# Performance work log

Hardware: AMD Instinct MI355X
Metric: run time of the kernel (lower is better)

The kernel has to match this reference:

```python
import jax, jax.numpy as jnp
import numpy as np

# Phi-3-small blocksparse config
S = 2048            # num prompt tokens (single sequence)
H = 32              # num query heads
HKV = 8             # num kv heads (GQA)
D = 128             # head size
BLK = 64            # sparse_block_size
LOCAL = 16          # local_blocks
VERT = 8            # vert_stride
SCALE = 0.08838834764831845  # 1/sqrt(128)
HEAD_SLIDE = max(1, VERT // H)  # = 1 (per-head vertical offset, homo_head=False)


def _blocksparse_mask():
    """Per-head local+strided block-sparse causal mask, shape [H, S, S] bool."""
    nb = S // BLK
    qb = jnp.arange(nb)[None, :, None]   # query block idx
    kb = jnp.arange(nb)[None, None, :]   # key block idx
    h = jnp.arange(H)[:, None, None]
    blk = (qb >= kb) & (
        (qb - kb < LOCAL) | (((kb + h * HEAD_SLIDE + 1) % VERT) == 0)
    )  # [H, nb, nb]
    dense = jnp.repeat(jnp.repeat(blk, BLK, axis=1), BLK, axis=2)  # [H, S, S]
    causal = jnp.arange(S)[:, None] >= jnp.arange(S)[None, :]
    return dense & causal[None]


def setup_inputs() -> dict:
    key = jax.random.key(0)
    k1, k2, k3 = jax.random.split(key, 3)
    return {
        "query": jax.random.normal(k1, (S, H * D), dtype=jnp.float32),
        "key": jax.random.normal(k2, (S, HKV * D), dtype=jnp.float32),
        "value": jax.random.normal(k3, (S, HKV * D), dtype=jnp.float32),
    }


def reference(query, key, value):
    q = query.reshape(S, H, D)
    k = jnp.repeat(key.reshape(S, HKV, D), H // HKV, axis=1)    # GQA expand
    v = jnp.repeat(value.reshape(S, HKV, D), H // HKV, axis=1)
    scores = jnp.einsum("qhd,khd->hqk", q, k) * SCALE           # [H, S, S]
    mask = _blocksparse_mask()
    scores = jnp.where(mask, scores, jnp.finfo(scores.dtype).min)
    p = jax.nn.softmax(scores, axis=-1)
    out = jnp.einsum("hqk,khd->qhd", p, v)                      # [S, H, D]
    return out.reshape(S, H * D)
```

## Files before the change

kernel.cpp:

```cpp
#include <hip/hip_runtime.h>


typedef __bf16 bf16_t;
typedef __bf16 bf16x4 __attribute__((ext_vector_type(4)));
typedef __bf16 bf16x8 __attribute__((ext_vector_type(8)));
typedef float  fx4    __attribute__((ext_vector_type(4)));

#define SL2E_F 0.1275240614354876f

__device__ inline void load_lds16(const bf16_t* g, bf16_t* l) {
    __builtin_amdgcn_global_load_lds(
        (const __attribute__((address_space(1))) void*)g,
        (__attribute__((address_space(3))) void*)l, 16, 0, 0);
}

__global__ void prep_kernel(const float* __restrict__ K, const float* __restrict__ V,
                            bf16_t* __restrict__ Kb, bf16_t* __restrict__ VT)
{
    const int blk = blockIdx.x;
    {
        const size_t base = (size_t)blk * 4096 + (size_t)threadIdx.x * 16;
        fx4 a0 = *(const fx4*)(K + base);
        fx4 a1 = *(const fx4*)(K + base + 4);
        fx4 a2 = *(const fx4*)(K + base + 8);
        fx4 a3 = *(const fx4*)(K + base + 12);
        bf16x8 f0, f1;
        f0[0]=(bf16_t)a0[0]; f0[1]=(bf16_t)a0[1]; f0[2]=(bf16_t)a0[2]; f0[3]=(bf16_t)a0[3];
        f0[4]=(bf16_t)a1[0]; f0[5]=(bf16_t)a1[1]; f0[6]=(bf16_t)a1[2]; f0[7]=(bf16_t)a1[3];
        f1[0]=(bf16_t)a2[0]; f1[1]=(bf16_t)a2[1]; f1[2]=(bf16_t)a2[2]; f1[3]=(bf16_t)a2[3];
        f1[4]=(bf16_t)a3[0]; f1[5]=(bf16_t)a3[1]; f1[6]=(bf16_t)a3[2]; f1[7]=(bf16_t)a3[3];
        *(bf16x8*)(Kb + base)     = f0;
        *(bf16x8*)(Kb + base + 8) = f1;
    }
    __shared__ __align__(16) bf16_t T[64 * 72];
    const int s0 = (blk & 31) * 64;
    const int c0 = (blk >> 5) * 64;
    const int tx = threadIdx.x & 15, ty = threadIdx.x >> 4;
    fx4 a0 = *(const fx4*)(V + (size_t)(s0 + ty * 4 + 0) * 1024 + c0 + tx * 4);
    fx4 a1 = *(const fx4*)(V + (size_t)(s0 + ty * 4 + 1) * 1024 + c0 + tx * 4);
    fx4 a2 = *(const fx4*)(V + (size_t)(s0 + ty * 4 + 2) * 1024 + c0 + tx * 4);
    fx4 a3 = *(const fx4*)(V + (size_t)(s0 + ty * 4 + 3) * 1024 + c0 + tx * 4);
#pragma unroll
    for (int j = 0; j < 4; ++j) {
        bf16x4 f = { (bf16_t)a0[j], (bf16_t)a1[j], (bf16_t)a2[j], (bf16_t)a3[j] };
        *(bf16x4*)&T[(tx * 4 + j) * 72 + ty * 4] = f;
    }
    __syncthreads();
    const int c = threadIdx.x >> 2, part = threadIdx.x & 3;
    bf16x8 x0 = *(const bf16x8*)&T[c * 72 + part * 16];
    bf16x8 x1 = *(const bf16x8*)&T[c * 72 + part * 16 + 8];
    bf16_t* dst = VT + (size_t)(c0 + c) * 2048 + s0 + part * 16;
    *(bf16x8*)(dst)     = x0;
    *(bf16x8*)(dst + 8) = x1;
}

__launch_bounds__(128, 2)
__global__ void bsfa_kernel(const float* __restrict__ Q,
                            const bf16_t* __restrict__ Kb,
                            const bf16_t* __restrict__ VT,
                            float* __restrict__ O)
{
    const int blk  = blockIdx.x;
    const int kvh  = blk & 7;
    const int h    = kvh * 4 + ((blk >> 3) & 3);
    const int qb   = 31 - (blk >> 5);
    const int tid  = threadIdx.x;
    const int rh   = tid >> 6;
    const int lane = tid & 63;
    const int l15  = lane & 15;
    const int quad = lane >> 4;

    __shared__ __align__(16) bf16_t Ks[64 * 128];
    __shared__ __align__(16) bf16_t Vs[128 * 64];

    bf16_t* Pt = &Ks[rh * 2304];

    const int row0 = qb * 64 + rh * 32;

    const bf16_t* kg = Kb + (size_t)kvh * 128;
    const bf16_t* vg = VT + ((size_t)kvh * 128) * 2048;

    bf16x8 qf[2][4];
#pragma unroll
    for (int qt = 0; qt < 2; ++qt) {
        const float* qp = Q + (size_t)(row0 + qt * 16 + l15) * 4096 + h * 128;
#pragma unroll
        for (int kc = 0; kc < 4; ++kc) {
            fx4 a = *(const fx4*)(qp + kc * 32 + quad * 8);
            fx4 b = *(const fx4*)(qp + kc * 32 + quad * 8 + 4);
            bf16x8 f;
            f[0] = (bf16_t)(a[0] * SL2E_F); f[1] = (bf16_t)(a[1] * SL2E_F);
            f[2] = (bf16_t)(a[2] * SL2E_F); f[3] = (bf16_t)(a[3] * SL2E_F);
            f[4] = (bf16_t)(b[0] * SL2E_F); f[5] = (bf16_t)(b[1] * SL2E_F);
            f[6] = (bf16_t)(b[2] * SL2E_F); f[7] = (bf16_t)(b[3] * SL2E_F);
            qf[qt][kc] = f;
        }
    }

    bf16x8 ones;
#pragma unroll
    for (int i = 0; i < 8; ++i) ones[i] = (bf16_t)1.0f;

    fx4 oacc[8][2];
    fx4 lacc[2];
    const fx4 zero4 = {0.0f, 0.0f, 0.0f, 0.0f};
#pragma unroll
    for (int dt = 0; dt < 8; ++dt)
#pragma unroll
        for (int qt = 0; qt < 2; ++qt)
            oacc[dt][qt] = zero4;
    lacc[0] = zero4; lacc[1] = zero4;

    for (int kb = 0; kb <= qb; ++kb) {
        if (!((qb - kb < 16) || (((kb + h + 1) & 7) == 0))) continue;

        {
            const bf16_t* kt_g = kg + ((size_t)kb << 16);
            const bf16_t* vt_g = vg + ((size_t)kb << 6);
#pragma unroll
            for (int i = 0; i < 8; ++i) {
                const int chunk = i * 128 + tid;
                const int krow = chunk >> 4;
                const int kc   = (chunk & 15) ^ (krow & 15);
                load_lds16(kt_g + (size_t)krow * 1024 + kc * 8, Ks + (size_t)chunk * 8);
                const int vrow = chunk >> 3;
                const int vc   = (chunk & 7) ^ (vrow & 7);
                load_lds16(vt_g + (size_t)vrow * 2048 + vc * 8, Vs + (size_t)chunk * 8);
            }
        }
        __syncthreads();

        fx4 sacc[4][2];
#pragma unroll
        for (int kt = 0; kt < 4; ++kt)
#pragma unroll
            for (int qt = 0; qt < 2; ++qt)
                sacc[kt][qt] = zero4;
#pragma unroll
        for (int kc = 0; kc < 4; ++kc)
#pragma unroll
            for (int kt = 0; kt < 4; ++kt) {
                bf16x8 kf = *(const bf16x8*)&Ks[(kt * 16 + l15) * 128 + (((kc * 4 + quad) ^ l15)) * 8];
#pragma unroll
                for (int qt = 0; qt < 2; ++qt)
                    sacc[kt][qt] = __builtin_amdgcn_mfma_f32_16x16x32_bf16(
                        kf, qf[qt][kc], sacc[kt][qt], 0, 0, 0);
            }

        if (kb == qb) {
#pragma unroll
            for (int kt = 0; kt < 4; ++kt)
#pragma unroll
                for (int qt = 0; qt < 2; ++qt)
#pragma unroll
                    for (int r = 0; r < 4; ++r) {
                        const int k_in = kt * 16 + quad * 4 + r;
                        const int q_in = rh * 32 + qt * 16 + l15;
                        if (q_in < k_in) sacc[kt][qt][r] = -1e30f;
                    }
        }

#pragma unroll
        for (int kt = 0; kt < 4; ++kt)
#pragma unroll
            for (int qt = 0; qt < 2; ++qt)
#pragma unroll
                for (int r = 0; r < 4; ++r)
                    sacc[kt][qt][r] = exp2f(sacc[kt][qt][r]);

        __syncthreads();

#pragma unroll
        for (int qt = 0; qt < 2; ++qt)
#pragma unroll
            for (int kt = 0; kt < 4; ++kt) {
                bf16x4 f = { (bf16_t)sacc[kt][qt][0], (bf16_t)sacc[kt][qt][1],
                             (bf16_t)sacc[kt][qt][2], (bf16_t)sacc[kt][qt][3] };
                *(bf16x4*)&Pt[(qt * 16 + l15) * 72 + kt * 16 + quad * 4] = f;
            }
        __asm__ __volatile__("s_waitcnt lgkmcnt(0)" ::: "memory");

        bf16x8 pf[2][2];
#pragma unroll
        for (int qt = 0; qt < 2; ++qt)
#pragma unroll
            for (int kcg = 0; kcg < 2; ++kcg)
                pf[qt][kcg] = *(const bf16x8*)&Pt[(qt * 16 + l15) * 72 + kcg * 32 + quad * 8];

#pragma unroll
        for (int kcg = 0; kcg < 2; ++kcg) {
#pragma unroll
            for (int dt = 0; dt < 8; ++dt) {
                bf16x8 vf = *(const bf16x8*)&Vs[(dt * 16 + l15) * 64 + (((kcg * 4 + quad) ^ (l15 & 7))) * 8];
#pragma unroll
                for (int qt = 0; qt < 2; ++qt)
                    oacc[dt][qt] = __builtin_amdgcn_mfma_f32_16x16x32_bf16(
                        vf, pf[qt][kcg], oacc[dt][qt], 0, 0, 0);
            }
#pragma unroll
            for (int qt = 0; qt < 2; ++qt)
                lacc[qt] = __builtin_amdgcn_mfma_f32_16x16x32_bf16(
                    ones, pf[qt][kcg], lacc[qt], 0, 0, 0);
        }

        __syncthreads();
    }

    const float inv0 = 1.0f / lacc[0][0];
    const float inv1 = 1.0f / lacc[1][0];
#pragma unroll
    for (int dt = 0; dt < 8; ++dt)
#pragma unroll
        for (int qt = 0; qt < 2; ++qt) {
            const float inv = qt ? inv1 : inv0;
            fx4 o = oacc[dt][qt] * inv;
            *(fx4*)(O + (size_t)(row0 + qt * 16 + l15) * 4096 + h * 128 + dt * 16 + quad * 4) = o;
        }
}

extern "C" void kernel_launch(void* const* d_in, const int* in_sizes, int n_in,
                              void* d_out, int out_size, void* d_ws, size_t ws_size,
                              hipStream_t stream) {
    (void)in_sizes; (void)n_in; (void)ws_size; (void)out_size;
    const float* q = (const float*)d_in[0];
    const float* k = (const float*)d_in[1];
    const float* v = (const float*)d_in[2];
    float* o = (float*)d_out;

    bf16_t* Kb = (bf16_t*)d_ws;
    bf16_t* VT = Kb + (size_t)2048 * 1024;

    prep_kernel<<<dim3(512), dim3(256), 0, stream>>>(k, v, Kb, VT);
    bsfa_kernel<<<dim3(1024), dim3(128), 0, stream>>>(q, Kb, VT, o);
}
```

Before: 138.7 us.

## Share K/V tiles across four load-balanced query blocks with double-buffered LDS

Each workgroup now has four waves, each owning a full 64-row query block chosen as x, 15-x, 16+x, 31-x so causal work is balanced. K/V tiles for the union of needed key blocks are staged once into double-buffered LDS and prefetched ahead of compute, which cuts redundant global loads. The P operand is rearranged in registers with permlane swaps instead of an LDS round trip. In exchange the grid drops to 256 workgroups with heavy register use (larger accumulators), which risks low occupancy and idle waves on tiles another wave needs.

```diff
diff --git a/kernel.cpp b/kernel.cpp
--- a/kernel.cpp
+++ b/kernel.cpp
@@ -5,6 +5,8 @@
 typedef __bf16 bf16x4 __attribute__((ext_vector_type(4)));
 typedef __bf16 bf16x8 __attribute__((ext_vector_type(8)));
 typedef float  fx4    __attribute__((ext_vector_type(4)));
+typedef unsigned u32x2 __attribute__((ext_vector_type(2)));
+typedef unsigned u32x4 __attribute__((ext_vector_type(4)));
 
 #define SL2E_F 0.1275240614354876f
 
@@ -12,6 +14,17 @@
     __builtin_amdgcn_global_load_lds(
         (const __attribute__((address_space(1))) void*)g,
         (__attribute__((address_space(3))) void*)l, 16, 0, 0);
+}
+
+__device__ inline unsigned cvt_pk_bf16(float lo, float hi) {
+    unsigned r;
+    asm("v_cvt_pk_bf16_f32 %0, %1, %2" : "=v"(r) : "v"(lo), "v"(hi));
+    return r;
+}
+
+__device__ inline u32x2 quad_gather(unsigned A) {
+    u32x2 bc = __builtin_amdgcn_permlane32_swap(A, A, false, false);
+    return __builtin_amdgcn_permlane16_swap(bc[0], bc[1], false, false);
 }
 
 __global__ void prep_kernel(const float* __restrict__ K, const float* __restrict__ V,
@@ -54,7 +67,7 @@
     *(bf16x8*)(dst + 8) = x1;
 }
 
-__launch_bounds__(128, 2)
+__launch_bounds__(256, 1)
 __global__ void bsfa_kernel(const float* __restrict__ Q,
                             const bf16_t* __restrict__ Kb,
                             const bf16_t* __restrict__ VT,
@@ -62,27 +75,30 @@
 {
     const int blk  = blockIdx.x;
     const int kvh  = blk & 7;
-    const int h    = kvh * 4 + ((blk >> 3) & 3);
-    const int qb   = 31 - (blk >> 5);
+    const int hsub = (blk >> 3) & 3;
+    const int x    = blk >> 5;
+    const int h    = kvh * 4 + hsub;
     const int tid  = threadIdx.x;
-    const int rh   = tid >> 6;
+    const int w    = tid >> 6;
     const int lane = tid & 63;
     const int l15  = lane & 15;
     const int quad = lane >> 4;
-
-    __shared__ __align__(16) bf16_t Ks[64 * 128];
-    __shared__ __align__(16) bf16_t Vs[128 * 64];
-
-    bf16_t* Pt = &Ks[rh * 2304];
-
-    const int row0 = qb * 64 + rh * 32;
+    const bool hi32 = (lane >= 32);
+
+    const int qb   = (w == 0) ? x : (w == 1) ? (15 - x) : (w == 2) ? (16 + x) : (31 - x);
+    const int qA   = x, qB = 15 - x, qC = 16 + x, qD = 31 - x;
+    const int qmax = qD;
+
+    __shared__ __align__(16) bf16_t Ks[2][64 * 128];
+    __shared__ __align__(16) bf16_t Vs[2][128 * 64];
 
     const bf16_t* kg = Kb + (size_t)kvh * 128;
     const bf16_t* vg = VT + ((size_t)kvh * 128) * 2048;
 
-    bf16x8 qf[2][4];
-#pragma unroll
-    for (int qt = 0; qt < 2; ++qt) {
+    const int row0 = qb * 64;
+    bf16x8 qf[4][4];
+#pragma unroll
+    for (int qt = 0; qt < 4; ++qt) {
         const float* qp = Q + (size_t)(row0 + qt * 16 + l15) * 4096 + h * 128;
 #pragma unroll
         for (int kc = 0; kc < 4; ++kc) {
@@ -101,121 +117,143 @@
 #pragma unroll
     for (int i = 0; i < 8; ++i) ones[i] = (bf16_t)1.0f;
 
-    fx4 oacc[8][2];
-    fx4 lacc[2];
+    fx4 oacc[8][4];
+    fx4 lacc[4];
     const fx4 zero4 = {0.0f, 0.0f, 0.0f, 0.0f};
 #pragma unroll
     for (int dt = 0; dt < 8; ++dt)
 #pragma unroll
-        for (int qt = 0; qt < 2; ++qt)
-            oacc[dt][qt] = zero4;
-    lacc[0] = zero4; lacc[1] = zero4;
-
-    for (int kb = 0; kb <= qb; ++kb) {
-        if (!((qb - kb < 16) || (((kb + h + 1) & 7) == 0))) continue;
-
-        {
-            const bf16_t* kt_g = kg + ((size_t)kb << 16);
-            const bf16_t* vt_g = vg + ((size_t)kb << 6);
-#pragma unroll
-            for (int i = 0; i < 8; ++i) {
-                const int chunk = i * 128 + tid;
-                const int krow = chunk >> 4;
-                const int kc   = (chunk & 15) ^ (krow & 15);
-                load_lds16(kt_g + (size_t)krow * 1024 + kc * 8, Ks + (size_t)chunk * 8);
-                const int vrow = chunk >> 3;
-                const int vc   = (chunk & 7) ^ (vrow & 7);
-                load_lds16(vt_g + (size_t)vrow * 2048 + vc * 8, Vs + (size_t)chunk * 8);
+        for (int qt = 0; qt < 4; ++qt) oacc[dt][qt] = zero4;
+#pragma unroll
+    for (int qt = 0; qt < 4; ++qt) lacc[qt] = zero4;
+
+    auto stage = [&](int kb, int bi) {
+        const bf16_t* kt_g = kg + ((size_t)kb << 16);
+        const bf16_t* vt_g = vg + ((size_t)kb << 6);
+        bf16_t* kd = &Ks[bi][0];
+        bf16_t* vd = &Vs[bi][0];
+#pragma unroll
+        for (int i = 0; i < 4; ++i) {
+            const int chunk = i * 256 + tid;
+            const int krow  = chunk >> 4;
+            const int kc    = (chunk & 15) ^ (krow & 15);
+            load_lds16(kt_g + (size_t)krow * 1024 + kc * 8, kd + (size_t)chunk * 8);
+            const int vrow  = chunk >> 3;
+            const int vc    = (chunk & 7) ^ (vrow & 7);
+            load_lds16(vt_g + (size_t)vrow * 2048 + vc * 8, vd + (size_t)chunk * 8);
+        }
+    };
+
+    stage(0, 0);
+    __syncthreads();
+
+    int kb = 0, cur = 0;
+    while (kb >= 0) {
+        int nkb = -1;
+        for (int t = kb + 1; t <= qmax; ++t) {
+            const bool st  = ((t + h + 1) & 7) == 0;
+            const bool any = st ? true
+                : ((t <= qA) ||
+                   (t <= qB && qB - t < 16) ||
+                   (t <= qC && qC - t < 16) ||
+                   (t <= qD && qD - t < 16));
+            if (any) { nkb = t; break; }
+        }
+        if (nkb >= 0) stage(nkb, cur ^ 1);
+
+        const bool act = (kb <= qb) && ((qb - kb < 16) || (((kb + h + 1) & 7) == 0));
+        if (act) {
+            const bf16_t* kd = &Ks[cur][0];
+            const bf16_t* vd = &Vs[cur][0];
+
+            fx4 sacc[4][4];
+#pragma unroll
+            for (int kt = 0; kt < 4; ++kt)
+#pragma unroll
+                for (int qt = 0; qt < 4; ++qt) sacc[kt][qt] = zero4;
+#pragma unroll
+            for (int kc = 0; kc < 4; ++kc)
+#pragma unroll
+                for (int kt = 0; kt < 4; ++kt) {
+                    bf16x8 kf = *(const bf16x8*)&kd[(kt * 16 + l15) * 128 + ((kc * 4 + quad) ^ l15) * 8];
+#pragma unroll
+                    for (int qt = 0; qt < 4; ++qt)
+                        sacc[kt][qt] = __builtin_amdgcn_mfma_f32_16x16x32_bf16(
+                            kf, qf[qt][kc], sacc[kt][qt], 0, 0, 0);
+                }
+
+            if (kb == qb) {
+#pragma unroll
+                for (int kt = 0; kt < 4; ++kt)
+#pragma unroll
+                    for (int qt = 0; qt < 4; ++qt)
+#pragma unroll
+                        for (int r = 0; r < 4; ++r) {
+                            const int k_in = kt * 16 + quad * 4 + r;
+                            const int q_in = qt * 16 + l15;
+                            if (q_in < k_in) sacc[kt][qt][r] = -1e30f;
+                        }
             }
-        }
+
+#pragma unroll
+            for (int kt = 0; kt < 4; ++kt)
+#pragma unroll
+                for (int qt = 0; qt < 4; ++qt)
+#pragma unroll
+                    for (int r = 0; r < 4; ++r)
+                        sacc[kt][qt][r] = exp2f(sacc[kt][qt][r]);
+
+            bf16x8 pf[4][2];
+#pragma unroll
+            for (int qt = 0; qt < 4; ++qt)
+#pragma unroll
+                for (int kcg = 0; kcg < 2; ++kcg) {
+                    const unsigned a00 = cvt_pk_bf16(sacc[2*kcg  ][qt][0], sacc[2*kcg  ][qt][1]);
+                    const unsigned a01 = cvt_pk_bf16(sacc[2*kcg  ][qt][2], sacc[2*kcg  ][qt][3]);
+                    const unsigned a10 = cvt_pk_bf16(sacc[2*kcg+1][qt][0], sacc[2*kcg+1][qt][1]);
+                    const unsigned a11 = cvt_pk_bf16(sacc[2*kcg+1][qt][2], sacc[2*kcg+1][qt][3]);
+                    const u32x2 g00 = quad_gather(a00);
+                    const u32x2 g01 = quad_gather(a01);
+                    const u32x2 g10 = quad_gather(a10);
+                    const u32x2 g11 = quad_gather(a11);
+                    u32x4 pw;
+                    pw[0] = hi32 ? g10[0] : g00[0];
+                    pw[1] = hi32 ? g11[0] : g01[0];
+                    pw[2] = hi32 ? g10[1] : g00[1];
+                    pw[3] = hi32 ? g11[1] : g01[1];
+                    pf[qt][kcg] = __builtin_bit_cast(bf16x8, pw);
+                }
+
+#pragma unroll
+            for (int kcg = 0; kcg < 2; ++kcg) {
+#pragma unroll
+                for (int dt = 0; dt < 8; ++dt) {
+                    bf16x8 vf = *(const bf16x8*)&vd[(dt * 16 + l15) * 64 + ((kcg * 4 + quad) ^ (l15 & 7)) * 8];
+#pragma unroll
+                    for (int qt = 0; qt < 4; ++qt)
+                        oacc[dt][qt] = __builtin_amdgcn_mfma_f32_16x16x32_bf16(
+                            vf, pf[qt][kcg], oacc[dt][qt], 0, 0, 0);
+                }
+#pragma unroll
+                for (int qt = 0; qt < 4; ++qt)
+                    lacc[qt] = __builtin_amdgcn_mfma_f32_16x16x32_bf16(
+                        ones, pf[qt][kcg], lacc[qt], 0, 0, 0);
+            }
+        }
+
         __syncthreads();
-
-        fx4 sacc[4][2];
-#pragma unroll
-        for (int kt = 0; kt < 4; ++kt)
-#pragma unroll
-            for (int qt = 0; qt < 2; ++qt)
-                sacc[kt][qt] = zero4;
-#pragma unroll
-        for (int kc = 0; kc < 4; ++kc)
-#pragma unroll
-            for (int kt = 0; kt < 4; ++kt) {
-                bf16x8 kf = *(const bf16x8*)&Ks[(kt * 16 + l15) * 128 + (((kc * 4 + quad) ^ l15)) * 8];
-#pragma unroll
-                for (int qt = 0; qt < 2; ++qt)
-                    sacc[kt][qt] = __builtin_amdgcn_mfma_f32_16x16x32_bf16(
-                        kf, qf[qt][kc], sacc[kt][qt], 0, 0, 0);
-            }
-
-        if (kb == qb) {
-#pragma unroll
-            for (int kt = 0; kt < 4; ++kt)
-#pragma unroll
-                for (int qt = 0; qt < 2; ++qt)
-#pragma unroll
-                    for (int r = 0; r < 4; ++r) {
-                        const int k_in = kt * 16 + quad * 4 + r;
-                        const int q_in = rh * 32 + qt * 16 + l15;
-                        if (q_in < k_in) sacc[kt][qt][r] = -1e30f;
-                    }
-        }
-
-#pragma unroll
-        for (int kt = 0; kt < 4; ++kt)
-#pragma unroll
-            for (int qt = 0; qt < 2; ++qt)
-#pragma unroll
-                for (int r = 0; r < 4; ++r)
-                    sacc[kt][qt][r] = exp2f(sacc[kt][qt][r]);
-
-        __syncthreads();
-
-#pragma unroll
-        for (int qt = 0; qt < 2; ++qt)
-#pragma unroll
-            for (int kt = 0; kt < 4; ++kt) {
-                bf16x4 f = { (bf16_t)sacc[kt][qt][0], (bf16_t)sacc[kt][qt][1],
-                             (bf16_t)sacc[kt][qt][2], (bf16_t)sacc[kt][qt][3] };
-                *(bf16x4*)&Pt[(qt * 16 + l15) * 72 + kt * 16 + quad * 4] = f;
-            }
-        __asm__ __volatile__("s_waitcnt lgkmcnt(0)" ::: "memory");
-
-        bf16x8 pf[2][2];
-#pragma unroll
-        for (int qt = 0; qt < 2; ++qt)
-#pragma unroll
-            for (int kcg = 0; kcg < 2; ++kcg)
-                pf[qt][kcg] = *(const bf16x8*)&Pt[(qt * 16 + l15) * 72 + kcg * 32 + quad * 8];
-
-#pragma unroll
-        for (int kcg = 0; kcg < 2; ++kcg) {
-#pragma unroll
-            for (int dt = 0; dt < 8; ++dt) {
-                bf16x8 vf = *(const bf16x8*)&Vs[(dt * 16 + l15) * 64 + (((kcg * 4 + quad) ^ (l15 & 7))) * 8];
-#pragma unroll
-                for (int qt = 0; qt < 2; ++qt)
-                    oacc[dt][qt] = __builtin_amdgcn_mfma_f32_16x16x32_bf16(
-                        vf, pf[qt][kcg], oacc[dt][qt], 0, 0, 0);
-            }
-#pragma unroll
-            for (int qt = 0; qt < 2; ++qt)
-                lacc[qt] = __builtin_amdgcn_mfma_f32_16x16x32_bf16(
-                    ones, pf[qt][kcg], lacc[qt], 0, 0, 0);
-        }
-
-        __syncthreads();
-    }
-
-    const float inv0 = 1.0f / lacc[0][0];
-    const float inv1 = 1.0f / lacc[1][0];
-#pragma unroll
-    for (int dt = 0; dt < 8; ++dt)
-#pragma unroll
-        for (int qt = 0; qt < 2; ++qt) {
-            const float inv = qt ? inv1 : inv0;
+        kb = nkb; cur ^= 1;
+    }
+
+#pragma unroll
+    for (int qt = 0; qt < 4; ++qt) {
+        const float inv = 1.0f / lacc[qt][0];
+#pragma unroll
+        for (int dt = 0; dt < 8; ++dt) {
             fx4 o = oacc[dt][qt] * inv;
             *(fx4*)(O + (size_t)(row0 + qt * 16 + l15) * 4096 + h * 128 + dt * 16 + quad * 4) = o;
         }
+    }
 }
 
 extern "C" void kernel_launch(void* const* d_in, const int* in_sizes, int n_in,
@@ -231,5 +269,5 @@
     bf16_t* VT = Kb + (size_t)2048 * 1024;
 
     prep_kernel<<<dim3(512), dim3(256), 0, stream>>>(k, v, Kb, VT);
-    bsfa_kernel<<<dim3(1024), dim3(128), 0, stream>>>(q, Kb, VT, o);
-}
+    bsfa_kernel<<<dim3(256), dim3(256), 0, stream>>>(q, Kb, VT, o);
+}
```

Result: slower. 197.1 us (+42.1%).

## Double-buffer K/V tiles, iterate only active blocks, and keep P in registers via permlane

Applied to the files above, without the earlier changes.

Doubles the LDS K/V buffers so the next active key block is prefetched with async global-to-LDS loads while the current one is computed. The loop now walks only the strided and local blocks directly instead of testing every block up to qb. P is converted with packed bf16 conversion and rearranged across lanes with permlane swaps, which drops the LDS round-trip and one barrier per iteration. Doubling LDS to 64KB and relaxing launch bounds to one block lowers occupancy and may increase register pressure.

```diff
diff --git a/kernel.cpp b/kernel.cpp
--- a/kernel.cpp
+++ b/kernel.cpp
@@ -5,6 +5,8 @@
 typedef __bf16 bf16x4 __attribute__((ext_vector_type(4)));
 typedef __bf16 bf16x8 __attribute__((ext_vector_type(8)));
 typedef float  fx4    __attribute__((ext_vector_type(4)));
+typedef unsigned u32x2 __attribute__((ext_vector_type(2)));
+typedef unsigned u32x4 __attribute__((ext_vector_type(4)));
 
 #define SL2E_F 0.1275240614354876f
 
@@ -12,6 +14,17 @@
     __builtin_amdgcn_global_load_lds(
         (const __attribute__((address_space(1))) void*)g,
         (__attribute__((address_space(3))) void*)l, 16, 0, 0);
+}
+
+__device__ inline unsigned cvt_pk_bf16(float lo, float hi) {
+    unsigned r;
+    asm("v_cvt_pk_bf16_f32 %0, %1, %2" : "=v"(r) : "v"(lo), "v"(hi));
+    return r;
+}
+
+__device__ inline u32x2 quad_gather(unsigned A) {
+    u32x2 bc = __builtin_amdgcn_permlane32_swap(A, A, false, false);
+    return __builtin_amdgcn_permlane16_swap(bc[0], bc[1], false, false);
 }
 
 __global__ void prep_kernel(const float* __restrict__ K, const float* __restrict__ V,
@@ -54,7 +67,7 @@
     *(bf16x8*)(dst + 8) = x1;
 }
 
-__launch_bounds__(128, 2)
+__launch_bounds__(128, 1)
 __global__ void bsfa_kernel(const float* __restrict__ Q,
                             const bf16_t* __restrict__ Kb,
                             const bf16_t* __restrict__ VT,
@@ -69,11 +82,10 @@
     const int lane = tid & 63;
     const int l15  = lane & 15;
     const int quad = lane >> 4;
-
-    __shared__ __align__(16) bf16_t Ks[64 * 128];
-    __shared__ __align__(16) bf16_t Vs[128 * 64];
-
-    bf16_t* Pt = &Ks[rh * 2304];
+    const bool hi32 = (lane >= 32);
+
+    __shared__ __align__(16) bf16_t Ks[2][64 * 128];
+    __shared__ __align__(16) bf16_t Vs[2][128 * 64];
 
     const int row0 = qb * 64 + rh * 32;
 
@@ -107,40 +119,55 @@
 #pragma unroll
     for (int dt = 0; dt < 8; ++dt)
 #pragma unroll
-        for (int qt = 0; qt < 2; ++qt)
-            oacc[dt][qt] = zero4;
+        for (int qt = 0; qt < 2; ++qt) oacc[dt][qt] = zero4;
     lacc[0] = zero4; lacc[1] = zero4;
 
-    for (int kb = 0; kb <= qb; ++kb) {
-        if (!((qb - kb < 16) || (((kb + h + 1) & 7) == 0))) continue;
-
-        {
-            const bf16_t* kt_g = kg + ((size_t)kb << 16);
-            const bf16_t* vt_g = vg + ((size_t)kb << 6);
-#pragma unroll
-            for (int i = 0; i < 8; ++i) {
-                const int chunk = i * 128 + tid;
-                const int krow = chunk >> 4;
-                const int kc   = (chunk & 15) ^ (krow & 15);
-                load_lds16(kt_g + (size_t)krow * 1024 + kc * 8, Ks + (size_t)chunk * 8);
-                const int vrow = chunk >> 3;
-                const int vc   = (chunk & 7) ^ (vrow & 7);
-                load_lds16(vt_g + (size_t)vrow * 2048 + vc * 8, Vs + (size_t)chunk * 8);
-            }
-        }
-        __syncthreads();
+    auto stage = [&](int kb, int bi) {
+        const bf16_t* kt_g = kg + ((size_t)kb << 16);
+        const bf16_t* vt_g = vg + ((size_t)kb << 6);
+        bf16_t* kd = &Ks[bi][0];
+        bf16_t* vd = &Vs[bi][0];
+#pragma unroll
+        for (int i = 0; i < 8; ++i) {
+            const int chunk = i * 128 + tid;
+            const int krow = chunk >> 4;
+            const int kc   = (chunk & 15) ^ (krow & 15);
+            load_lds16(kt_g + (size_t)krow * 1024 + kc * 8, kd + (size_t)chunk * 8);
+            const int vrow = chunk >> 3;
+            const int vc   = (chunk & 7) ^ (vrow & 7);
+            load_lds16(vt_g + (size_t)vrow * 2048 + vc * 8, vd + (size_t)chunk * 8);
+        }
+    };
+
+    const int loc0 = (qb > 15) ? (qb - 15) : 0;
+    const int kb0s = (8 - ((h + 1) & 7)) & 7;
+    auto nxt = [&](int kb) -> int {
+        if (kb < loc0) { const int t = kb + 8; return (t <= qb - 16) ? t : loc0; }
+        return (kb < qb) ? (kb + 1) : -1;
+    };
+
+    int kb = (qb - 16 >= kb0s) ? kb0s : loc0;
+    stage(kb, 0);
+    __syncthreads();
+
+    int cur = 0;
+    while (kb >= 0) {
+        const int nkb = nxt(kb);
+        if (nkb >= 0) stage(nkb, cur ^ 1);
+
+        const bf16_t* kd = &Ks[cur][0];
+        const bf16_t* vd = &Vs[cur][0];
 
         fx4 sacc[4][2];
 #pragma unroll
         for (int kt = 0; kt < 4; ++kt)
 #pragma unroll
-            for (int qt = 0; qt < 2; ++qt)
-                sacc[kt][qt] = zero4;
+            for (int qt = 0; qt < 2; ++qt) sacc[kt][qt] = zero4;
 #pragma unroll
         for (int kc = 0; kc < 4; ++kc)
 #pragma unroll
             for (int kt = 0; kt < 4; ++kt) {
-                bf16x8 kf = *(const bf16x8*)&Ks[(kt * 16 + l15) * 128 + (((kc * 4 + quad) ^ l15)) * 8];
+                bf16x8 kf = *(const bf16x8*)&kd[(kt * 16 + l15) * 128 + ((kc * 4 + quad) ^ l15) * 8];
 #pragma unroll
                 for (int qt = 0; qt < 2; ++qt)
                     sacc[kt][qt] = __builtin_amdgcn_mfma_f32_16x16x32_bf16(
@@ -168,30 +195,32 @@
                 for (int r = 0; r < 4; ++r)
                     sacc[kt][qt][r] = exp2f(sacc[kt][qt][r]);
 
-        __syncthreads();
-
+        bf16x8 pf[2][2];
 #pragma unroll
         for (int qt = 0; qt < 2; ++qt)
 #pragma unroll
-            for (int kt = 0; kt < 4; ++kt) {
-                bf16x4 f = { (bf16_t)sacc[kt][qt][0], (bf16_t)sacc[kt][qt][1],
-                             (bf16_t)sacc[kt][qt][2], (bf16_t)sacc[kt][qt][3] };
-                *(bf16x4*)&Pt[(qt * 16 + l15) * 72 + kt * 16 + quad * 4] = f;
+            for (int kcg = 0; kcg < 2; ++kcg) {
+                const unsigned a00 = cvt_pk_bf16(sacc[2*kcg  ][qt][0], sacc[2*kcg  ][qt][1]);
+                const unsigned a01 = cvt_pk_bf16(sacc[2*kcg  ][qt][2], sacc[2*kcg  ][qt][3]);
+                const unsigned a10 = cvt_pk_bf16(sacc[2*kcg+1][qt][0], sacc[2*kcg+1][qt][1]);
+                const unsigned a11 = cvt_pk_bf16(sacc[2*kcg+1][qt][2], sacc[2*kcg+1][qt][3]);
+                const u32x2 g00 = quad_gather(a00);
+                const u32x2 g01 = quad_gather(a01);
+                const u32x2 g10 = quad_gather(a10);
+                const u32x2 g11 = quad_gather(a11);
+                u32x4 pw;
+                pw[0] = hi32 ? g10[0] : g00[0];
+                pw[1] = hi32 ? g11[0] : g01[0];
+                pw[2] = hi32 ? g10[1] : g00[1];
+                pw[3] = hi32 ? g11[1] : g01[1];
+                pf[qt][kcg] = __builtin_bit_cast(bf16x8, pw);
             }
-        __asm__ __volatile__("s_waitcnt lgkmcnt(0)" ::: "memory");
-
-        bf16x8 pf[2][2];
-#pragma unroll
-        for (int qt = 0; qt < 2; ++qt)
-#pragma unroll
-            for (int kcg = 0; kcg < 2; ++kcg)
-                pf[qt][kcg] = *(const bf16x8*)&Pt[(qt * 16 + l15) * 72 + kcg * 32 + quad * 8];
 
 #pragma unroll
         for (int kcg = 0; kcg < 2; ++kcg) {
 #pragma unroll
             for (int dt = 0; dt < 8; ++dt) {
-                bf16x8 vf = *(const bf16x8*)&Vs[(dt * 16 + l15) * 64 + (((kcg * 4 + quad) ^ (l15 & 7))) * 8];
+                bf16x8 vf = *(const bf16x8*)&vd[(dt * 16 + l15) * 64 + ((kcg * 4 + quad) ^ (l15 & 7)) * 8];
 #pragma unroll
                 for (int qt = 0; qt < 2; ++qt)
                     oacc[dt][qt] = __builtin_amdgcn_mfma_f32_16x16x32_bf16(
@@ -204,18 +233,18 @@
         }
 
         __syncthreads();
-    }
-
-    const float inv0 = 1.0f / lacc[0][0];
-    const float inv1 = 1.0f / lacc[1][0];
-#pragma unroll
-    for (int dt = 0; dt < 8; ++dt)
-#pragma unroll
-        for (int qt = 0; qt < 2; ++qt) {
-            const float inv = qt ? inv1 : inv0;
+        kb = nkb; cur ^= 1;
+    }
+
+#pragma unroll
+    for (int qt = 0; qt < 2; ++qt) {
+        const float inv = 1.0f / lacc[qt][0];
+#pragma unroll
+        for (int dt = 0; dt < 8; ++dt) {
             fx4 o = oacc[dt][qt] * inv;
             *(fx4*)(O + (size_t)(row0 + qt * 16 + l15) * 4096 + h * 128 + dt * 16 + quad * 4) = o;
         }
+    }
 }
 
 extern "C" void kernel_launch(void* const* d_in, const int* in_sizes, int n_in,
```

New measurement: 164.6 us. +18.7%, slower.

## Split KV blocks across waves with per-wave LDS prefetch and merge

Applied to the files above, without the earlier changes.

Each of the two waves now owns all 64 query rows and handles alternating key blocks, which it walks directly through a next-block iterator instead of testing every block. Each wave has its own K/V LDS buffer, issues the next block's loads before its PV MFMAs, and uses waitcnt in place of block-wide barriers. The partial outputs and row sums are combined through LDS at the end. The change doubles accumulator registers, lowers the occupancy hint to one block, and adds a final merge pass.

```diff
diff --git a/kernel.cpp b/kernel.cpp
--- a/kernel.cpp
+++ b/kernel.cpp
@@ -54,7 +54,7 @@
     *(bf16x8*)(dst + 8) = x1;
 }
 
-__launch_bounds__(128, 2)
+__launch_bounds__(128, 1)
 __global__ void bsfa_kernel(const float* __restrict__ Q,
                             const bf16_t* __restrict__ Kb,
                             const bf16_t* __restrict__ VT,
@@ -65,24 +65,53 @@
     const int h    = kvh * 4 + ((blk >> 3) & 3);
     const int qb   = 31 - (blk >> 5);
     const int tid  = threadIdx.x;
-    const int rh   = tid >> 6;
+    const int w    = tid >> 6;
     const int lane = tid & 63;
     const int l15  = lane & 15;
     const int quad = lane >> 4;
 
-    __shared__ __align__(16) bf16_t Ks[64 * 128];
-    __shared__ __align__(16) bf16_t Vs[128 * 64];
-
-    bf16_t* Pt = &Ks[rh * 2304];
-
-    const int row0 = qb * 64 + rh * 32;
+    __shared__ __align__(16) bf16_t SMEM[2][16384];
+    __shared__ float Lmerge[64];
+
+    bf16_t* Ksw = &SMEM[w][0];
+    bf16_t* Vsw = &SMEM[w][8192];
+    bf16_t* Pt  = Ksw;
+
+    const int row0 = qb * 64;
 
     const bf16_t* kg = Kb + (size_t)kvh * 128;
     const bf16_t* vg = VT + ((size_t)kvh * 128) * 2048;
 
-    bf16x8 qf[2][4];
-#pragma unroll
-    for (int qt = 0; qt < 2; ++qt) {
+    const int loc0 = (qb > 15) ? (qb - 15) : 0;
+    const int kb0s = (8 - ((h + 1) & 7)) & 7;
+    auto nxt = [&](int kb) -> int {
+        if (kb < loc0) { const int t = kb + 8; return (t <= qb - 16) ? t : loc0; }
+        return (kb < qb) ? (kb + 1) : -1;
+    };
+
+    int kb = (qb - 16 >= kb0s) ? kb0s : loc0;
+    if (w == 1) kb = nxt(kb);
+
+    auto stage = [&](int t) {
+        const bf16_t* kt_g = kg + ((size_t)t << 16);
+        const bf16_t* vt_g = vg + ((size_t)t << 6);
+#pragma unroll
+        for (int i = 0; i < 16; ++i) {
+            const int chunk = i * 64 + lane;
+            const int krow = chunk >> 4;
+            const int kc   = (chunk & 15) ^ (krow & 15);
+            load_lds16(kt_g + (size_t)krow * 1024 + kc * 8, Ksw + (size_t)chunk * 8);
+            const int vrow = chunk >> 3;
+            const int vc   = (chunk & 7) ^ (vrow & 7);
+            load_lds16(vt_g + (size_t)vrow * 2048 + vc * 8, Vsw + (size_t)chunk * 8);
+        }
+    };
+
+    if (kb >= 0) stage(kb);
+
+    bf16x8 qf[4][4];
+#pragma unroll
+    for (int qt = 0; qt < 4; ++qt) {
         const float* qp = Q + (size_t)(row0 + qt * 16 + l15) * 4096 + h * 128;
 #pragma unroll
         for (int kc = 0; kc < 4; ++kc) {
@@ -101,48 +130,35 @@
 #pragma unroll
     for (int i = 0; i < 8; ++i) ones[i] = (bf16_t)1.0f;
 
-    fx4 oacc[8][2];
-    fx4 lacc[2];
+    fx4 oacc[8][4];
+    fx4 lacc[4];
     const fx4 zero4 = {0.0f, 0.0f, 0.0f, 0.0f};
 #pragma unroll
     for (int dt = 0; dt < 8; ++dt)
 #pragma unroll
-        for (int qt = 0; qt < 2; ++qt)
-            oacc[dt][qt] = zero4;
-    lacc[0] = zero4; lacc[1] = zero4;
-
-    for (int kb = 0; kb <= qb; ++kb) {
-        if (!((qb - kb < 16) || (((kb + h + 1) & 7) == 0))) continue;
-
-        {
-            const bf16_t* kt_g = kg + ((size_t)kb << 16);
-            const bf16_t* vt_g = vg + ((size_t)kb << 6);
-#pragma unroll
-            for (int i = 0; i < 8; ++i) {
-                const int chunk = i * 128 + tid;
-                const int krow = chunk >> 4;
-                const int kc   = (chunk & 15) ^ (krow & 15);
-                load_lds16(kt_g + (size_t)krow * 1024 + kc * 8, Ks + (size_t)chunk * 8);
-                const int vrow = chunk >> 3;
-                const int vc   = (chunk & 7) ^ (vrow & 7);
-                load_lds16(vt_g + (size_t)vrow * 2048 + vc * 8, Vs + (size_t)chunk * 8);
-            }
-        }
-        __syncthreads();
-
-        fx4 sacc[4][2];
+        for (int qt = 0; qt < 4; ++qt) oacc[dt][qt] = zero4;
+#pragma unroll
+    for (int qt = 0; qt < 4; ++qt) lacc[qt] = zero4;
+
+    while (kb >= 0) {
+        int nkb = nxt(kb);
+        if (nkb >= 0) nkb = nxt(nkb);
+
+        asm volatile("s_waitcnt vmcnt(0)" ::: "memory");
+        __builtin_amdgcn_sched_barrier(0);
+
+        fx4 sacc[4][4];
 #pragma unroll
         for (int kt = 0; kt < 4; ++kt)
 #pragma unroll
-            for (int qt = 0; qt < 2; ++qt)
-                sacc[kt][qt] = zero4;
+            for (int qt = 0; qt < 4; ++qt) sacc[kt][qt] = zero4;
 #pragma unroll
         for (int kc = 0; kc < 4; ++kc)
 #pragma unroll
             for (int kt = 0; kt < 4; ++kt) {
-                bf16x8 kf = *(const bf16x8*)&Ks[(kt * 16 + l15) * 128 + (((kc * 4 + quad) ^ l15)) * 8];
-#pragma unroll
-                for (int qt = 0; qt < 2; ++qt)
+                bf16x8 kf = *(const bf16x8*)&Ksw[(kt * 16 + l15) * 128 + ((kc * 4 + quad) ^ l15) * 8];
+#pragma unroll
+                for (int qt = 0; qt < 4; ++qt)
                     sacc[kt][qt] = __builtin_amdgcn_mfma_f32_16x16x32_bf16(
                         kf, qf[qt][kc], sacc[kt][qt], 0, 0, 0);
             }
@@ -151,11 +167,11 @@
 #pragma unroll
             for (int kt = 0; kt < 4; ++kt)
 #pragma unroll
-                for (int qt = 0; qt < 2; ++qt)
+                for (int qt = 0; qt < 4; ++qt)
 #pragma unroll
                     for (int r = 0; r < 4; ++r) {
                         const int k_in = kt * 16 + quad * 4 + r;
-                        const int q_in = rh * 32 + qt * 16 + l15;
+                        const int q_in = qt * 16 + l15;
                         if (q_in < k_in) sacc[kt][qt][r] = -1e30f;
                     }
         }
@@ -163,59 +179,84 @@
 #pragma unroll
         for (int kt = 0; kt < 4; ++kt)
 #pragma unroll
-            for (int qt = 0; qt < 2; ++qt)
+            for (int qt = 0; qt < 4; ++qt)
 #pragma unroll
                 for (int r = 0; r < 4; ++r)
                     sacc[kt][qt][r] = exp2f(sacc[kt][qt][r]);
 
-        __syncthreads();
-
-#pragma unroll
-        for (int qt = 0; qt < 2; ++qt)
+        asm volatile("s_waitcnt lgkmcnt(0)" ::: "memory");
+        __builtin_amdgcn_sched_barrier(0);
+#pragma unroll
+        for (int qt = 0; qt < 4; ++qt)
 #pragma unroll
             for (int kt = 0; kt < 4; ++kt) {
                 bf16x4 f = { (bf16_t)sacc[kt][qt][0], (bf16_t)sacc[kt][qt][1],
                              (bf16_t)sacc[kt][qt][2], (bf16_t)sacc[kt][qt][3] };
                 *(bf16x4*)&Pt[(qt * 16 + l15) * 72 + kt * 16 + quad * 4] = f;
             }
-        __asm__ __volatile__("s_waitcnt lgkmcnt(0)" ::: "memory");
-
-        bf16x8 pf[2][2];
-#pragma unroll
-        for (int qt = 0; qt < 2; ++qt)
+        asm volatile("s_waitcnt lgkmcnt(0)" ::: "memory");
+        __builtin_amdgcn_sched_barrier(0);
+
+        bf16x8 pf[4][2];
+#pragma unroll
+        for (int qt = 0; qt < 4; ++qt)
 #pragma unroll
             for (int kcg = 0; kcg < 2; ++kcg)
                 pf[qt][kcg] = *(const bf16x8*)&Pt[(qt * 16 + l15) * 72 + kcg * 32 + quad * 8];
+        bf16x8 vf[2][8];
+#pragma unroll
+        for (int kcg = 0; kcg < 2; ++kcg)
+#pragma unroll
+            for (int dt = 0; dt < 8; ++dt)
+                vf[kcg][dt] = *(const bf16x8*)&Vsw[(dt * 16 + l15) * 64 + ((kcg * 4 + quad) ^ (l15 & 7)) * 8];
+
+        asm volatile("s_waitcnt lgkmcnt(0)" ::: "memory");
+        __builtin_amdgcn_sched_barrier(0);
+        if (nkb >= 0) stage(nkb);
 
 #pragma unroll
         for (int kcg = 0; kcg < 2; ++kcg) {
 #pragma unroll
-            for (int dt = 0; dt < 8; ++dt) {
-                bf16x8 vf = *(const bf16x8*)&Vs[(dt * 16 + l15) * 64 + (((kcg * 4 + quad) ^ (l15 & 7))) * 8];
-#pragma unroll
-                for (int qt = 0; qt < 2; ++qt)
+            for (int dt = 0; dt < 8; ++dt)
+#pragma unroll
+                for (int qt = 0; qt < 4; ++qt)
                     oacc[dt][qt] = __builtin_amdgcn_mfma_f32_16x16x32_bf16(
-                        vf, pf[qt][kcg], oacc[dt][qt], 0, 0, 0);
-            }
-#pragma unroll
-            for (int qt = 0; qt < 2; ++qt)
+                        vf[kcg][dt], pf[qt][kcg], oacc[dt][qt], 0, 0, 0);
+#pragma unroll
+            for (int qt = 0; qt < 4; ++qt)
                 lacc[qt] = __builtin_amdgcn_mfma_f32_16x16x32_bf16(
                     ones, pf[qt][kcg], lacc[qt], 0, 0, 0);
         }
 
-        __syncthreads();
-    }
-
-    const float inv0 = 1.0f / lacc[0][0];
-    const float inv1 = 1.0f / lacc[1][0];
-#pragma unroll
-    for (int dt = 0; dt < 8; ++dt)
-#pragma unroll
-        for (int qt = 0; qt < 2; ++qt) {
-            const float inv = qt ? inv1 : inv0;
-            fx4 o = oacc[dt][qt] * inv;
-            *(fx4*)(O + (size_t)(row0 + qt * 16 + l15) * 4096 + h * 128 + dt * 16 + quad * 4) = o;
-        }
+        kb = nkb;
+    }
+
+    __syncthreads();
+    if (w == 1) {
+        float* Obuf = (float*)&SMEM[1][0];
+#pragma unroll
+        for (int dt = 0; dt < 8; ++dt)
+#pragma unroll
+            for (int qt = 0; qt < 4; ++qt)
+                *(fx4*)&Obuf[(((dt * 4 + qt) * 64) + lane) * 4] = oacc[dt][qt];
+        if (quad == 0) {
+#pragma unroll
+            for (int qt = 0; qt < 4; ++qt) Lmerge[qt * 16 + l15] = lacc[qt][0];
+        }
+    }
+    __syncthreads();
+    if (w == 0) {
+        const float* Obuf = (const float*)&SMEM[1][0];
+#pragma unroll
+        for (int qt = 0; qt < 4; ++qt) {
+            const float inv = 1.0f / (lacc[qt][0] + Lmerge[qt * 16 + l15]);
+#pragma unroll
+            for (int dt = 0; dt < 8; ++dt) {
+                fx4 o = (oacc[dt][qt] + *(const fx4*)&Obuf[(((dt * 4 + qt) * 64) + lane) * 4]) * inv;
+                *(fx4*)(O + (size_t)(row0 + qt * 16 + l15) * 4096 + h * 128 + dt * 16 + quad * 4) = o;
+            }
+        }
+    }
 }
 
 extern "C" void kernel_launch(void* const* d_in, const int* in_sizes, int n_in,
```

Result: slower. 210.6 us (+51.8%).
